# Performance work log

Hardware: AMD Instinct MI355X
Metric: run time of the kernel (lower is better)

The kernel has to match this reference:

```python
import jax, jax.numpy as jnp
import numpy as np

N, C, H, W_SP, E = 32, 64, 128, 128, 512


def setup_inputs() -> dict:
    key = jax.random.key(0)
    k1, k2, k3 = jax.random.split(key, 3)
    images = jax.random.normal(k1, (N, C, H, W_SP), dtype=jnp.float32)
    atts = jax.random.normal(k2, (N, E), dtype=jnp.float32)
    # nn.Linear(E, C*C): weight [C*C, E], bias [C*C]
    W = jax.random.normal(k3, (C * C, E), dtype=jnp.float32) * (1.0 / np.sqrt(E))
    b = jnp.zeros((C * C,), dtype=jnp.float32)
    return {"images": images, "atts": atts, "W": W, "b": b}


def reference(images, atts, W, b):
    n, c, h, w = images.shape
    logits = atts @ W.T + b                      # [N, C*C]
    a = jax.nn.softmax(logits, axis=-1)          # softmax over flattened C*C (first softmax)
    a = a.reshape(n, c, c)
    a = jax.nn.softmax(a, axis=-1)               # second softmax over last C (redundant but faithful)
    # out[n,c,h,w] = sum_d a[n,c,d] * images[n,d,h,w]  (batched [C,C]x[C,HW] matmul)
    out = jnp.einsum('ncd,ndhw->nchw', a, images)
    return out
```

## Files before the change

kernel.cpp:

```cpp
#include <hip/hip_runtime.h>
#include <hip/hip_bf16.h>

#define NB   32
#define CC   64
#define HW   16384
#define EE   512
#define CC2  4096

using short8  = __attribute__((ext_vector_type(8))) short;
using f32x16  = __attribute__((ext_vector_type(16))) float;

__device__ __forceinline__ unsigned short f2bf(float x) {
    unsigned int u = __float_as_uint(x);
    u += 0x7FFFu + ((u >> 16) & 1u);
    return (unsigned short)(u >> 16);
}

__global__ __launch_bounds__(256) void logits_kernel(
    const float* __restrict__ atts, const float* __restrict__ W,
    const float* __restrict__ b, float* __restrict__ logits) {
    const int t  = threadIdx.x;
    const int j  = blockIdx.x * 2 + (t & 1);
    const int n  = (t >> 1) & 31;
    const int kq = t >> 6;
    const float* __restrict__ wrow = W + (size_t)j * EE + kq * 128;
    const float* __restrict__ arow = atts + (size_t)n * EE + kq * 128;
    float acc0 = 0.f, acc1 = 0.f;
    #pragma unroll
    for (int k = 0; k < 128; k += 8) {
        float4 w0 = *reinterpret_cast<const float4*>(wrow + k);
        float4 a0 = *reinterpret_cast<const float4*>(arow + k);
        float4 w1 = *reinterpret_cast<const float4*>(wrow + k + 4);
        float4 a1 = *reinterpret_cast<const float4*>(arow + k + 4);
        acc0 = fmaf(w0.x, a0.x, acc0); acc0 = fmaf(w0.y, a0.y, acc0);
        acc0 = fmaf(w0.z, a0.z, acc0); acc0 = fmaf(w0.w, a0.w, acc0);
        acc1 = fmaf(w1.x, a1.x, acc1); acc1 = fmaf(w1.y, a1.y, acc1);
        acc1 = fmaf(w1.z, a1.z, acc1); acc1 = fmaf(w1.w, a1.w, acc1);
    }
    __shared__ float part[256];
    part[t] = acc0 + acc1;
    __syncthreads();
    if (t < 64) {
        const int jj = blockIdx.x * 2 + (t & 1);
        const int nn = t >> 1;
        const float r = part[t] + part[t + 64] + part[t + 128] + part[t + 192];
        logits[(size_t)nn * CC2 + jj] = r + b[jj];
    }
}

__global__ __launch_bounds__(256) void softmax_kernel(
    const float* __restrict__ logits, unsigned short* __restrict__ a_pk) {
    const int n = blockIdx.x;
    const int t = threadIdx.x;
    __shared__ float s[CC2];
    __shared__ float wmax[4];
    __shared__ float wsum[4];

    const float* __restrict__ L = logits + (size_t)n * CC2;

    float lmax = -1e30f;
    for (int i = t; i < CC2; i += 256) {
        float v = L[i];
        s[i] = v;
        lmax = fmaxf(lmax, v);
    }
    #pragma unroll
    for (int off = 32; off > 0; off >>= 1) lmax = fmaxf(lmax, __shfl_xor(lmax, off));
    if ((t & 63) == 0) wmax[t >> 6] = lmax;
    __syncthreads();
    const float bmax = fmaxf(fmaxf(wmax[0], wmax[1]), fmaxf(wmax[2], wmax[3]));

    float lsum = 0.f;
    for (int i = t; i < CC2; i += 256) {
        float e = __expf(s[i] - bmax);
        s[i] = e;
        lsum += e;
    }
    #pragma unroll
    for (int off = 32; off > 0; off >>= 1) lsum += __shfl_xor(lsum, off);
    if ((t & 63) == 0) wsum[t >> 6] = lsum;
    __syncthreads();
    const float inv = 1.f / (wsum[0] + wsum[1] + wsum[2] + wsum[3]);

    for (int i = t; i < CC2; i += 256) s[i] *= inv;
    __syncthreads();

    const int c = t >> 2;
    const int q = t & 3;
    const float* __restrict__ row = s + c * CC + q * 16;
    float mx = -1e30f;
    #pragma unroll
    for (int i = 0; i < 16; ++i) mx = fmaxf(mx, row[i]);
    mx = fmaxf(mx, __shfl_xor(mx, 1));
    mx = fmaxf(mx, __shfl_xor(mx, 2));
    float sum = 0.f;
    #pragma unroll
    for (int i = 0; i < 16; ++i) sum += __expf(row[i] - mx);
    sum += __shfl_xor(sum, 1);
    sum += __shfl_xor(sum, 2);
    const float isum = 1.f / sum;

    union { uint4 u[2]; unsigned short h[16]; } pk;
    #pragma unroll
    for (int i = 0; i < 16; ++i) pk.h[i] = f2bf(__expf(row[i] - mx) * isum);

    const int half = c >> 5;
    const int lc2  = c & 31;
    unsigned short* __restrict__ base =
        a_pk + (size_t)n * CC2 + (size_t)(q * 2 + half) * 512;
    *reinterpret_cast<uint4*>(base + lc2 * 8)        = pk.u[0];
    *reinterpret_cast<uint4*>(base + (32 + lc2) * 8) = pk.u[1];
}

__global__ __launch_bounds__(512, 4) void einsum_kernel(
    const float* __restrict__ img, const unsigned short* __restrict__ a_pk,
    float* __restrict__ out) {
    const int t    = threadIdx.x;
    const int lane = t & 63;
    const int wv   = t >> 6;
    const int n    = blockIdx.y;
    const int px0  = blockIdx.x * 256;
    const int lh   = lane >> 5;
    const int lc   = lane & 31;

    __shared__ unsigned short sImg[CC * 256];

    {
        const int px_l = (t & 63) * 4;
        const int d0   = (t >> 6) * 8;
        const float* __restrict__ gp = img + (size_t)n * (CC * HW) + px0 + px_l;
        float4 v0 = *reinterpret_cast<const float4*>(gp + (size_t)(d0 + 0) * HW);
        float4 v1 = *reinterpret_cast<const float4*>(gp + (size_t)(d0 + 1) * HW);
        float4 v2 = *reinterpret_cast<const float4*>(gp + (size_t)(d0 + 2) * HW);
        float4 v3 = *reinterpret_cast<const float4*>(gp + (size_t)(d0 + 3) * HW);
        float4 v4 = *reinterpret_cast<const float4*>(gp + (size_t)(d0 + 4) * HW);
        float4 v5 = *reinterpret_cast<const float4*>(gp + (size_t)(d0 + 5) * HW);
        float4 v6 = *reinterpret_cast<const float4*>(gp + (size_t)(d0 + 6) * HW);
        float4 v7 = *reinterpret_cast<const float4*>(gp + (size_t)(d0 + 7) * HW);
        union { uint2 u; unsigned short h[4]; } pk;
        #define STG(i, vv) \
            pk.h[0] = f2bf(vv.x); pk.h[1] = f2bf(vv.y); \
            pk.h[2] = f2bf(vv.z); pk.h[3] = f2bf(vv.w); \
            *reinterpret_cast<uint2*>(&sImg[(d0 + i) * 256 + px_l]) = pk.u;
        STG(0, v0) STG(1, v1) STG(2, v2) STG(3, v3)
        STG(4, v4) STG(5, v5) STG(6, v6) STG(7, v7)
        #undef STG
    }
    __syncthreads();

    const int px_w = wv * 32 + lc;
    const unsigned short* __restrict__ apn = a_pk + (size_t)n * CC2;

    f32x16 acc0 = {};
    f32x16 acc1 = {};

    #pragma unroll
    for (int ks = 0; ks < 4; ++ks) {
        const int kbase = ks * 16 + lh * 8;
        union { short8 v; unsigned short h[8]; } bf;
        #pragma unroll
        for (int e = 0; e < 8; ++e)
            bf.h[e] = sImg[(kbase + e) * 256 + px_w];
        short8 a0 = *reinterpret_cast<const short8*>(apn + (ks * 2 + 0) * 512 + lane * 8);
        short8 a1 = *reinterpret_cast<const short8*>(apn + (ks * 2 + 1) * 512 + lane * 8);
        acc0 = __builtin_amdgcn_mfma_f32_32x32x16_bf16(a0, bf.v, acc0, 0, 0, 0);
        acc1 = __builtin_amdgcn_mfma_f32_32x32x16_bf16(a1, bf.v, acc1, 0, 0, 0);
    }

    float* __restrict__ op = out + (size_t)n * (CC * HW) + px0 + px_w;
    #pragma unroll
    for (int r = 0; r < 16; ++r) {
        const int row = (r & 3) + 8 * (r >> 2) + 4 * lh;
        __builtin_nontemporal_store(acc0[r], op + (size_t)row * HW);
        __builtin_nontemporal_store(acc1[r], op + (size_t)(row + 32) * HW);
    }
}

extern "C" void kernel_launch(void* const* d_in, const int* in_sizes, int n_in,
                              void* d_out, int out_size, void* d_ws, size_t ws_size,
                              hipStream_t stream) {
    const float* images = (const float*)d_in[0];
    const float* atts   = (const float*)d_in[1];
    const float* W      = (const float*)d_in[2];
    const float* b      = (const float*)d_in[3];
    float* out = (float*)d_out;

    float* logits = (float*)d_ws;
    unsigned short* a_pk = (unsigned short*)(logits + NB * CC2);

    logits_kernel<<<CC2 / 2, 256, 0, stream>>>(atts, W, b, logits);
    softmax_kernel<<<NB, 256, 0, stream>>>(logits, a_pk);
    einsum_kernel<<<dim3(HW / 256, NB), 512, 0, stream>>>(images, a_pk, out);
}
```

Measured before the change: 84.22 us.

## Double-buffer channel halves in einsum and stage output through LDS for vector stores

The einsum kernel now handles 512 pixels per block instead of 256. It splits the 64 input channels into two halves, loading the second half from global memory while MFMAs run on the first. The A fragments are preloaded into registers, and the LDS rows are padded to avoid bank conflicts. Outputs are transposed through shared memory so each thread writes 16-byte nontemporal vector stores instead of scalar strided ones. The cost is more barriers, a larger LDS footprint (about 66KB), half as many blocks, and more register pressure.

```diff
diff --git a/kernel.cpp b/kernel.cpp
--- a/kernel.cpp
+++ b/kernel.cpp
@@ -6,9 +6,11 @@
 #define HW   16384
 #define EE   512
 #define CC2  4096
+#define SROW 520
 
 using short8  = __attribute__((ext_vector_type(8))) short;
 using f32x16  = __attribute__((ext_vector_type(16))) float;
+using f32x4   = __attribute__((ext_vector_type(4))) float;
 
 __device__ __forceinline__ unsigned short f2bf(float x) {
     unsigned int u = __float_as_uint(x);
@@ -112,6 +114,26 @@
     *reinterpret_cast<uint4*>(base + (32 + lc2) * 8) = pk.u[1];
 }
 
+template<int BUF, int H>
+__device__ __forceinline__ void compute_half(
+    const unsigned short* sImg, const short8* afrag, int lh, int pxw0, int pxw1,
+    f32x16& acc00, f32x16& acc01, f32x16& acc10, f32x16& acc11) {
+    #pragma unroll
+    for (int ksl = 0; ksl < 2; ++ksl) {
+        const unsigned short* sb = sImg + BUF * 32 * SROW + (ksl * 16) * SROW + lh * 8 * SROW;
+        union { short8 v; unsigned short sh[8]; } b0, b1;
+        #pragma unroll
+        for (int e = 0; e < 8; ++e) {
+            b0.sh[e] = sb[e * SROW + pxw0];
+            b1.sh[e] = sb[e * SROW + pxw1];
+        }
+        acc00 = __builtin_amdgcn_mfma_f32_32x32x16_bf16(afrag[(H*2+ksl)*2+0], b0.v, acc00, 0, 0, 0);
+        acc10 = __builtin_amdgcn_mfma_f32_32x32x16_bf16(afrag[(H*2+ksl)*2+1], b0.v, acc10, 0, 0, 0);
+        acc01 = __builtin_amdgcn_mfma_f32_32x32x16_bf16(afrag[(H*2+ksl)*2+0], b1.v, acc01, 0, 0, 0);
+        acc11 = __builtin_amdgcn_mfma_f32_32x32x16_bf16(afrag[(H*2+ksl)*2+1], b1.v, acc11, 0, 0, 0);
+    }
+}
+
 __global__ __launch_bounds__(512, 4) void einsum_kernel(
     const float* __restrict__ img, const unsigned short* __restrict__ a_pk,
     float* __restrict__ out) {
@@ -119,60 +141,96 @@
     const int lane = t & 63;
     const int wv   = t >> 6;
     const int n    = blockIdx.y;
-    const int px0  = blockIdx.x * 256;
+    const int px0  = blockIdx.x * 512;
     const int lh   = lane >> 5;
     const int lc   = lane & 31;
 
-    __shared__ unsigned short sImg[CC * 256];
+    __shared__ __align__(16) unsigned short sImg[2 * 32 * SROW];
+
+    const float* __restrict__ gbase = img + (size_t)n * (CC * HW) + px0;
+    const int px_l = (t & 127) * 4;
+    const int dgrp = t >> 7;
+
+    const unsigned short* __restrict__ apn = a_pk + (size_t)n * CC2;
+    short8 afrag[8];
+    #pragma unroll
+    for (int i = 0; i < 8; ++i)
+        afrag[i] = *reinterpret_cast<const short8*>(apn + i * 512 + lane * 8);
 
     {
-        const int px_l = (t & 63) * 4;
-        const int d0   = (t >> 6) * 8;
-        const float* __restrict__ gp = img + (size_t)n * (CC * HW) + px0 + px_l;
-        float4 v0 = *reinterpret_cast<const float4*>(gp + (size_t)(d0 + 0) * HW);
-        float4 v1 = *reinterpret_cast<const float4*>(gp + (size_t)(d0 + 1) * HW);
-        float4 v2 = *reinterpret_cast<const float4*>(gp + (size_t)(d0 + 2) * HW);
-        float4 v3 = *reinterpret_cast<const float4*>(gp + (size_t)(d0 + 3) * HW);
-        float4 v4 = *reinterpret_cast<const float4*>(gp + (size_t)(d0 + 4) * HW);
-        float4 v5 = *reinterpret_cast<const float4*>(gp + (size_t)(d0 + 5) * HW);
-        float4 v6 = *reinterpret_cast<const float4*>(gp + (size_t)(d0 + 6) * HW);
-        float4 v7 = *reinterpret_cast<const float4*>(gp + (size_t)(d0 + 7) * HW);
-        union { uint2 u; unsigned short h[4]; } pk;
-        #define STG(i, vv) \
-            pk.h[0] = f2bf(vv.x); pk.h[1] = f2bf(vv.y); \
-            pk.h[2] = f2bf(vv.z); pk.h[3] = f2bf(vv.w); \
-            *reinterpret_cast<uint2*>(&sImg[(d0 + i) * 256 + px_l]) = pk.u;
-        STG(0, v0) STG(1, v1) STG(2, v2) STG(3, v3)
-        STG(4, v4) STG(5, v5) STG(6, v6) STG(7, v7)
-        #undef STG
-    }
-    __syncthreads();
-
-    const int px_w = wv * 32 + lc;
-    const unsigned short* __restrict__ apn = a_pk + (size_t)n * CC2;
-
-    f32x16 acc0 = {};
-    f32x16 acc1 = {};
-
-    #pragma unroll
-    for (int ks = 0; ks < 4; ++ks) {
-        const int kbase = ks * 16 + lh * 8;
-        union { short8 v; unsigned short h[8]; } bf;
+        float4 v[8];
         #pragma unroll
-        for (int e = 0; e < 8; ++e)
-            bf.h[e] = sImg[(kbase + e) * 256 + px_w];
-        short8 a0 = *reinterpret_cast<const short8*>(apn + (ks * 2 + 0) * 512 + lane * 8);
-        short8 a1 = *reinterpret_cast<const short8*>(apn + (ks * 2 + 1) * 512 + lane * 8);
-        acc0 = __builtin_amdgcn_mfma_f32_32x32x16_bf16(a0, bf.v, acc0, 0, 0, 0);
-        acc1 = __builtin_amdgcn_mfma_f32_32x32x16_bf16(a1, bf.v, acc1, 0, 0, 0);
-    }
-
-    float* __restrict__ op = out + (size_t)n * (CC * HW) + px0 + px_w;
+        for (int j = 0; j < 8; ++j)
+            v[j] = *reinterpret_cast<const float4*>(gbase + (size_t)(dgrp * 8 + j) * HW + px_l);
+        #pragma unroll
+        for (int j = 0; j < 8; ++j) {
+            union { uint2 u; unsigned short h4[4]; } pk;
+            pk.h4[0] = f2bf(v[j].x); pk.h4[1] = f2bf(v[j].y);
+            pk.h4[2] = f2bf(v[j].z); pk.h4[3] = f2bf(v[j].w);
+            *reinterpret_cast<uint2*>(&sImg[(dgrp * 8 + j) * SROW + px_l]) = pk.u;
+        }
+    }
+    __syncthreads();
+
+    f32x16 acc00 = {}, acc01 = {}, acc10 = {}, acc11 = {};
+    const int pxw0 = wv * 64 + lc;
+    const int pxw1 = pxw0 + 32;
+
+    float4 v1[8];
+    #pragma unroll
+    for (int j = 0; j < 8; ++j)
+        v1[j] = *reinterpret_cast<const float4*>(gbase + (size_t)(32 + dgrp * 8 + j) * HW + px_l);
+
+    compute_half<0, 0>(sImg, afrag, lh, pxw0, pxw1, acc00, acc01, acc10, acc11);
+
+    #pragma unroll
+    for (int j = 0; j < 8; ++j) {
+        union { uint2 u; unsigned short h4[4]; } pk;
+        pk.h4[0] = f2bf(v1[j].x); pk.h4[1] = f2bf(v1[j].y);
+        pk.h4[2] = f2bf(v1[j].z); pk.h4[3] = f2bf(v1[j].w);
+        *reinterpret_cast<uint2*>(&sImg[32 * SROW + (dgrp * 8 + j) * SROW + px_l]) = pk.u;
+    }
+    __syncthreads();
+
+    compute_half<1, 1>(sImg, afrag, lh, pxw0, pxw1, acc00, acc01, acc10, acc11);
+    __syncthreads();
+
+    float* sOut = reinterpret_cast<float*>(sImg);
+    float* __restrict__ obase = out + (size_t)n * (CC * HW) + px0;
+
     #pragma unroll
     for (int r = 0; r < 16; ++r) {
         const int row = (r & 3) + 8 * (r >> 2) + 4 * lh;
-        __builtin_nontemporal_store(acc0[r], op + (size_t)row * HW);
-        __builtin_nontemporal_store(acc1[r], op + (size_t)(row + 32) * HW);
+        sOut[row * 512 + pxw0] = acc00[r];
+        sOut[row * 512 + pxw1] = acc01[r];
+    }
+    __syncthreads();
+    #pragma unroll
+    for (int k = 0; k < 8; ++k) {
+        const int f4  = t + k * 512;
+        const int row = f4 >> 7;
+        const int px4 = f4 & 127;
+        const f32x4 val = reinterpret_cast<const f32x4*>(sOut)[f4];
+        __builtin_nontemporal_store(val,
+            reinterpret_cast<f32x4*>(obase + (size_t)row * HW + px4 * 4));
+    }
+    __syncthreads();
+
+    #pragma unroll
+    for (int r = 0; r < 16; ++r) {
+        const int row = (r & 3) + 8 * (r >> 2) + 4 * lh;
+        sOut[row * 512 + pxw0] = acc10[r];
+        sOut[row * 512 + pxw1] = acc11[r];
+    }
+    __syncthreads();
+    #pragma unroll
+    for (int k = 0; k < 8; ++k) {
+        const int f4  = t + k * 512;
+        const int row = f4 >> 7;
+        const int px4 = f4 & 127;
+        const f32x4 val = reinterpret_cast<const f32x4*>(sOut)[f4];
+        __builtin_nontemporal_store(val,
+            reinterpret_cast<f32x4*>(obase + (size_t)(row + 32) * HW + px4 * 4));
     }
 }
 
@@ -190,5 +248,5 @@
 
     logits_kernel<<<CC2 / 2, 256, 0, stream>>>(atts, W, b, logits);
     softmax_kernel<<<NB, 256, 0, stream>>>(logits, a_pk);
-    einsum_kernel<<<dim3(HW / 256, NB), 512, 0, stream>>>(images, a_pk, out);
-}
+    einsum_kernel<<<dim3(HW / 512, NB), 512, 0, stream>>>(images, a_pk, out);
+}
```

Measured after the change: 87.41 us. 3.8% more time.

## Make einsum kernel persistent over 4 pixel tiles with double-buffered LDS prefetch

Applied to the files above, without the earlier changes.

Each einsum block now handles 1024 pixels in four 256-pixel steps instead of one tile, so the grid drops from 2048 to 512 blocks. The next tile's global loads are issued into registers while the current tile is being computed. LDS uses two buffers with a padded row stride of 260 to cut bank conflicts. The A fragments are loaded once per block and reused across all four tiles. The cost is fewer blocks to spread across CUs and higher register and LDS use, which may lower occupancy.

```diff
diff --git a/kernel.cpp b/kernel.cpp
--- a/kernel.cpp
+++ b/kernel.cpp
@@ -6,6 +6,7 @@
 #define HW   16384
 #define EE   512
 #define CC2  4096
+#define SR2  260
 
 using short8  = __attribute__((ext_vector_type(8))) short;
 using f32x16  = __attribute__((ext_vector_type(16))) float;
@@ -118,61 +119,73 @@
     const int t    = threadIdx.x;
     const int lane = t & 63;
     const int wv   = t >> 6;
-    const int n    = blockIdx.y;
-    const int px0  = blockIdx.x * 256;
     const int lh   = lane >> 5;
     const int lc   = lane & 31;
 
-    __shared__ unsigned short sImg[CC * 256];
-
-    {
-        const int px_l = (t & 63) * 4;
-        const int d0   = (t >> 6) * 8;
-        const float* __restrict__ gp = img + (size_t)n * (CC * HW) + px0 + px_l;
-        float4 v0 = *reinterpret_cast<const float4*>(gp + (size_t)(d0 + 0) * HW);
-        float4 v1 = *reinterpret_cast<const float4*>(gp + (size_t)(d0 + 1) * HW);
-        float4 v2 = *reinterpret_cast<const float4*>(gp + (size_t)(d0 + 2) * HW);
-        float4 v3 = *reinterpret_cast<const float4*>(gp + (size_t)(d0 + 3) * HW);
-        float4 v4 = *reinterpret_cast<const float4*>(gp + (size_t)(d0 + 4) * HW);
-        float4 v5 = *reinterpret_cast<const float4*>(gp + (size_t)(d0 + 5) * HW);
-        float4 v6 = *reinterpret_cast<const float4*>(gp + (size_t)(d0 + 6) * HW);
-        float4 v7 = *reinterpret_cast<const float4*>(gp + (size_t)(d0 + 7) * HW);
-        union { uint2 u; unsigned short h[4]; } pk;
-        #define STG(i, vv) \
-            pk.h[0] = f2bf(vv.x); pk.h[1] = f2bf(vv.y); \
-            pk.h[2] = f2bf(vv.z); pk.h[3] = f2bf(vv.w); \
-            *reinterpret_cast<uint2*>(&sImg[(d0 + i) * 256 + px_l]) = pk.u;
-        STG(0, v0) STG(1, v1) STG(2, v2) STG(3, v3)
-        STG(4, v4) STG(5, v5) STG(6, v6) STG(7, v7)
-        #undef STG
-    }
-    __syncthreads();
-
-    const int px_w = wv * 32 + lc;
+    const int n      = blockIdx.x >> 4;
+    const int px_blk = (blockIdx.x & 15) * 1024;
+
+    __shared__ __align__(16) unsigned short sB[2 * CC * SR2];
+
+    const float* __restrict__ gbase = img + (size_t)n * (CC * HW);
     const unsigned short* __restrict__ apn = a_pk + (size_t)n * CC2;
 
-    f32x16 acc0 = {};
-    f32x16 acc1 = {};
-
-    #pragma unroll
-    for (int ks = 0; ks < 4; ++ks) {
-        const int kbase = ks * 16 + lh * 8;
-        union { short8 v; unsigned short h[8]; } bf;
+    const int srow = t >> 6;
+    const int scol = (t & 63) * 4;
+
+    float4 v[8];
+    #pragma unroll
+    for (int i = 0; i < 8; ++i)
+        v[i] = *reinterpret_cast<const float4*>(
+            gbase + (size_t)(srow + i * 8) * HW + px_blk + scol);
+
+    short8 afrag[8];
+    #pragma unroll
+    for (int i = 0; i < 8; ++i)
+        afrag[i] = *reinterpret_cast<const short8*>(apn + i * 512 + lane * 8);
+
+    int buf = 0;
+    for (int it = 0; it < 4; ++it) {
+        const int px0 = px_blk + it * 256;
+
+        unsigned short* __restrict__ dst = sB + buf * (CC * SR2);
         #pragma unroll
-        for (int e = 0; e < 8; ++e)
-            bf.h[e] = sImg[(kbase + e) * 256 + px_w];
-        short8 a0 = *reinterpret_cast<const short8*>(apn + (ks * 2 + 0) * 512 + lane * 8);
-        short8 a1 = *reinterpret_cast<const short8*>(apn + (ks * 2 + 1) * 512 + lane * 8);
-        acc0 = __builtin_amdgcn_mfma_f32_32x32x16_bf16(a0, bf.v, acc0, 0, 0, 0);
-        acc1 = __builtin_amdgcn_mfma_f32_32x32x16_bf16(a1, bf.v, acc1, 0, 0, 0);
-    }
-
-    float* __restrict__ op = out + (size_t)n * (CC * HW) + px0 + px_w;
-    #pragma unroll
-    for (int r = 0; r < 16; ++r) {
-        const int row = (r & 3) + 8 * (r >> 2) + 4 * lh;
-        __builtin_nontemporal_store(acc0[r], op + (size_t)row * HW);
-        __builtin_nontemporal_store(acc1[r], op + (size_t)(row + 32) * HW);
+        for (int i = 0; i < 8; ++i) {
+            union { uint2 u; unsigned short h4[4]; } pk;
+            pk.h4[0] = f2bf(v[i].x); pk.h4[1] = f2bf(v[i].y);
+            pk.h4[2] = f2bf(v[i].z); pk.h4[3] = f2bf(v[i].w);
+            *reinterpret_cast<uint2*>(&dst[(srow + i * 8) * SR2 + scol]) = pk.u;
+        }
+
+        if (it < 3) {
+            #pragma unroll
+            for (int i = 0; i < 8; ++i)
+                v[i] = *reinterpret_cast<const float4*>(
+                    gbase + (size_t)(srow + i * 8) * HW + px_blk + (it + 1) * 256 + scol);
+        }
+        __syncthreads();
+
+        f32x16 acc0 = {}, acc1 = {};
+        const unsigned short* __restrict__ sb = sB + buf * (CC * SR2);
+        const int pxw = wv * 32 + lc;
+        #pragma unroll
+        for (int ks = 0; ks < 4; ++ks) {
+            union { short8 vv; unsigned short sh[8]; } b;
+            #pragma unroll
+            for (int e = 0; e < 8; ++e)
+                b.sh[e] = sb[(ks * 16 + lh * 8 + e) * SR2 + pxw];
+            acc0 = __builtin_amdgcn_mfma_f32_32x32x16_bf16(afrag[ks * 2 + 0], b.vv, acc0, 0, 0, 0);
+            acc1 = __builtin_amdgcn_mfma_f32_32x32x16_bf16(afrag[ks * 2 + 1], b.vv, acc1, 0, 0, 0);
+        }
+
+        float* __restrict__ op = out + (size_t)n * (CC * HW) + px0 + pxw;
+        #pragma unroll
+        for (int r = 0; r < 16; ++r) {
+            const int row = (r & 3) + 8 * (r >> 2) + 4 * lh;
+            __builtin_nontemporal_store(acc0[r], op + (size_t)row * HW);
+            __builtin_nontemporal_store(acc1[r], op + (size_t)(row + 32) * HW);
+        }
+        buf ^= 1;
     }
 }
 
@@ -190,5 +203,5 @@
 
     logits_kernel<<<CC2 / 2, 256, 0, stream>>>(atts, W, b, logits);
     softmax_kernel<<<NB, 256, 0, stream>>>(logits, a_pk);
-    einsum_kernel<<<dim3(HW / 256, NB), 512, 0, stream>>>(images, a_pk, out);
-}
+    einsum_kernel<<<NB * 16, 512, 0, stream>>>(images, a_pk, out);
+}
```

After: 129.3 us. 53.6% more time.
